# Performance work log

Measured on AMD Instinct MI355X. Metric: run time of the kernel, lower is better.

## Reference

```python
import jax, jax.numpy as jnp
import numpy as np

IN_F = 4096
OUT_F = 4096
N_TOK = 8192
MAX_ITER = IN_F * OUT_F // 2  # default max_iter=-1 -> half of weight entries


def _approx_matmul(x, weight, max_iter):
    """Budgeted approximate matmul: only the `max_iter` largest-magnitude
    weight entries participate (the rest of the multiply-accumulate budget is
    skipped). Faithful to the iteration-budget semantics of Approx_Matmul:
    max_iter multiply-adds out of in_features*out_features total.
    """
    n = weight.size
    flat_abs = jnp.abs(weight).reshape(-1)
    # threshold = k-th largest magnitude (static k -> jit-friendly)
    kth = jnp.sort(flat_abs)[n - max_iter]
    mask = (jnp.abs(weight) >= kth).astype(weight.dtype)
    w_eff = weight * jax.lax.stop_gradient(mask)
    # y[t, o] = sum_i x[t, i] * w_eff[o, i]
    return jnp.einsum('ti,oi->to', x, w_eff)


def setup_inputs() -> dict:
    key = jax.random.key(0)
    kx, kw, kb = jax.random.split(key, 3)
    x = jax.random.normal(kx, (N_TOK, IN_F), dtype=jnp.float32)
    # kaiming_uniform_(a=sqrt(5)) on [out, in] -> bound = 1/sqrt(in_features)
    bound = 1.0 / np.sqrt(IN_F)
    weight = jax.random.uniform(kw, (OUT_F, IN_F), dtype=jnp.float32,
                                minval=-bound, maxval=bound)
    bias = jax.random.uniform(kb, (OUT_F,), dtype=jnp.float32,
                              minval=-bound, maxval=bound)
    return {"x": x, "weight": weight, "bias": bias}


def reference(x, weight, bias):
    mid = _approx_matmul(x, weight, MAX_ITER)
    return mid + bias
```

## Files before the change

### kernel.cpp

```cpp
#include <hip/hip_runtime.h>

#define IN_F   4096
#define OUT_F  4096
#define N_TOK  8192
#define NW     (OUT_F * IN_F)
#define SEL_TARGET 8388608u
#define CAND_CAP (1u << 20)

#define LO_BITS 0x3BFCA000u
#define HI_BITS 0x3C018000u

typedef unsigned int  u32;
typedef unsigned short u16;

typedef __bf16 bf16x8 __attribute__((ext_vector_type(8)));
typedef float  f32x4  __attribute__((ext_vector_type(4)));
typedef u32    u32x4  __attribute__((ext_vector_type(4)));

__device__ inline u16 f2bf_rne(float f) {
    u32 u = __float_as_uint(f);
    u32 r = (u + 0x7fffu + ((u >> 16) & 1u)) >> 16;
    return (u16)r;
}

__global__ __launch_bounds__(256) void front_fused_kernel(
    const uint4* __restrict__ wb, const f32x4* __restrict__ xb,
    u32* __restrict__ cand, u16* __restrict__ x16,
    u32* __restrict__ scal) {
    if (blockIdx.x < 1024) {
        __shared__ u32 lbuf[4096];
        __shared__ u32 lcnt, gbase, lblw;
        if (threadIdx.x == 0) { lcnt = 0; lblw = 0; }
        __syncthreads();

        const int base = blockIdx.x * 4096;
        u32 cntb = 0;
        #pragma unroll 4
        for (int j = 0; j < 16; j++) {
            uint4 v = wb[base + threadIdx.x + j * 256];
            u32 k[4] = {v.x & 0x7fffffffu, v.y & 0x7fffffffu,
                        v.z & 0x7fffffffu, v.w & 0x7fffffffu};
            #pragma unroll
            for (int e = 0; e < 4; e++) {
                u32 kk = k[e];
                cntb += (kk < LO_BITS) ? 1u : 0u;
                if (kk >= LO_BITS && kk < HI_BITS) {
                    u32 idx = atomicAdd(&lcnt, 1u);
                    if (idx < 4096) lbuf[idx] = kk;
                    else scal[6] = 1u;
                }
            }
        }
        #pragma unroll
        for (int off = 32; off; off >>= 1) cntb += __shfl_down(cntb, off);
        if ((threadIdx.x & 63) == 0) atomicAdd(&lblw, cntb);
        __syncthreads();
        if (threadIdx.x == 0) {
            gbase = atomicAdd(&scal[3], min(lcnt, 4096u));
            atomicAdd(&scal[4], lblw);
        }
        __syncthreads();
        const u32 n = min(lcnt, 4096u), gb = gbase;
        for (u32 i = threadIdx.x; i < n; i += 256)
            if (gb + i < CAND_CAP) cand[gb + i] = lbuf[i];
    } else {
        const int stride = 2048 * 256;
        for (int i = (blockIdx.x - 1024) * 256 + threadIdx.x;
             i < (N_TOK * IN_F) / 4; i += stride) {
            f32x4 v = __builtin_nontemporal_load(&xb[i]);
            ushort4 o;
            o.x = f2bf_rne(v.x);
            o.y = f2bf_rne(v.y);
            o.z = f2bf_rne(v.z);
            o.w = f2bf_rne(v.w);
            *(ushort4*)&x16[(size_t)i * 4] = o;
        }
    }
}

#define SCAN1024(part, t)                                            \
    do { _Pragma("unroll")                                           \
        for (int off_ = 1; off_ < 1024; off_ <<= 1) {                \
            u32 v_ = ((t) >= off_) ? part[(t) - off_] : 0u;          \
            __syncthreads();                                         \
            part[t] += v_;                                           \
            __syncthreads();                                         \
        } } while (0)

__global__ __launch_bounds__(1024) void select_win_kernel(const u32* __restrict__ cand,
                                                          const uint4* __restrict__ wb,
                                                          u32* __restrict__ scal) {
    __shared__ u32 h[2048];
    __shared__ u32 part[1024];
    __shared__ u32 sh[2];
    const int t = threadIdx.x;
    const u32 n = scal[3], below = scal[4], ovf = scal[6];
    const bool valid = (n > 0) && (n <= CAND_CAP) && (ovf == 0) &&
                       (below <= SEL_TARGET) && (SEL_TARGET < below + n);

    if (valid) {
        u32 tgt = SEL_TARGET - below;
        const uint4* c4 = (const uint4*)cand;
        const u32 n4 = n >> 2;

        h[t] = 0; h[t + 1024] = 0;
        __syncthreads();
        for (u32 i = t; i < n4; i += 1024) {
            uint4 v = c4[i];
            atomicAdd(&h[(v.x - LO_BITS) >> 9], 1u);
            atomicAdd(&h[(v.y - LO_BITS) >> 9], 1u);
            atomicAdd(&h[(v.z - LO_BITS) >> 9], 1u);
            atomicAdd(&h[(v.w - LO_BITS) >> 9], 1u);
        }
        for (u32 i = (n4 << 2) + t; i < n; i += 1024)
            atomicAdd(&h[(cand[i] - LO_BITS) >> 9], 1u);
        __syncthreads();
        u32 c = h[t];
        part[t] = c;
        __syncthreads();
        SCAN1024(part, t);
        u32 cum = (t == 0) ? 0u : part[t - 1];
        if (tgt >= cum && tgt < cum + c) { sh[0] = (u32)t; sh[1] = tgt - cum; }
        __syncthreads();
        const u32 b1 = sh[0];
        tgt = sh[1];
        __syncthreads();

        h[t] = 0; h[t + 1024] = 0;
        __syncthreads();
        for (u32 i = t; i < n4; i += 1024) {
            uint4 v = c4[i];
            u32 d0 = v.x - LO_BITS, d1 = v.y - LO_BITS,
                d2 = v.z - LO_BITS, d3 = v.w - LO_BITS;
            if ((d0 >> 9) == b1) atomicAdd(&h[d0 & 511u], 1u);
            if ((d1 >> 9) == b1) atomicAdd(&h[d1 & 511u], 1u);
            if ((d2 >> 9) == b1) atomicAdd(&h[d2 & 511u], 1u);
            if ((d3 >> 9) == b1) atomicAdd(&h[d3 & 511u], 1u);
        }
        for (u32 i = (n4 << 2) + t; i < n; i += 1024) {
            u32 d = cand[i] - LO_BITS;
            if ((d >> 9) == b1) atomicAdd(&h[d & 511u], 1u);
        }
        __syncthreads();
        c = (t < 512) ? h[t] : 0u;
        part[t] = c;
        __syncthreads();
        SCAN1024(part, t);
        cum = (t == 0) ? 0u : part[t - 1];
        if (tgt >= cum && tgt < cum + c)
            scal[2] = LO_BITS + (b1 << 9) + (u32)t;
        return;
    }

    u32 tgt = SEL_TARGET;
    const int nvec = NW / 4;
    h[t] = 0; h[t + 1024] = 0;
    __syncthreads();
    for (int i = t; i < nvec; i += 1024) {
        uint4 v = wb[i];
        atomicAdd(&h[(v.x & 0x7fffffffu) >> 20], 1u);
        atomicAdd(&h[(v.y & 0x7fffffffu) >> 20], 1u);
        atomicAdd(&h[(v.z & 0x7fffffffu) >> 20], 1u);
        atomicAdd(&h[(v.w & 0x7fffffffu) >> 20], 1u);
    }
    __syncthreads();
    u32 a0 = h[2 * t], a1 = h[2 * t + 1];
    part[t] = a0 + a1;
    __syncthreads();
    SCAN1024(part, t);
    u32 cum = (t == 0) ? 0u : part[t - 1];
    if (tgt >= cum && tgt < cum + a0) { sh[0] = (u32)(2 * t);     sh[1] = tgt - cum; }
    cum += a0;
    if (tgt >= cum && tgt < cum + a1) { sh[0] = (u32)(2 * t + 1); sh[1] = tgt - cum; }
    __syncthreads();
    const u32 b1f = sh[0];
    tgt = sh[1];
    __syncthreads();

    h[t] = 0; h[t + 1024] = 0;
    __syncthreads();
    for (int i = t; i < nvec; i += 1024) {
        uint4 v = wb[i];
        u32 k[4] = {v.x & 0x7fffffffu, v.y & 0x7fffffffu,
                    v.z & 0x7fffffffu, v.w & 0x7fffffffu};
        #pragma unroll
        for (int e = 0; e < 4; e++)
            if ((k[e] >> 20) == b1f) atomicAdd(&h[(k[e] >> 9) & 2047u], 1u);
    }
    __syncthreads();
    a0 = h[2 * t]; a1 = h[2 * t + 1];
    part[t] = a0 + a1;
    __syncthreads();
    SCAN1024(part, t);
    cum = (t == 0) ? 0u : part[t - 1];
    if (tgt >= cum && tgt < cum + a0) { sh[0] = (u32)(2 * t);     sh[1] = tgt - cum; }
    cum += a0;
    if (tgt >= cum && tgt < cum + a1) { sh[0] = (u32)(2 * t + 1); sh[1] = tgt - cum; }
    __syncthreads();
    const u32 pfx22 = (b1f << 11) | sh[0];
    tgt = sh[1];
    __syncthreads();

    h[t] = 0; h[t + 1024] = 0;
    __syncthreads();
    for (int i = t; i < nvec; i += 1024) {
        uint4 v = wb[i];
        u32 k[4] = {v.x & 0x7fffffffu, v.y & 0x7fffffffu,
                    v.z & 0x7fffffffu, v.w & 0x7fffffffu};
        #pragma unroll
        for (int e = 0; e < 4; e++)
            if ((k[e] >> 9) == pfx22) atomicAdd(&h[k[e] & 511u], 1u);
    }
    __syncthreads();
    u32 c = (t < 512) ? h[t] : 0u;
    part[t] = c;
    __syncthreads();
    SCAN1024(part, t);
    cum = (t == 0) ? 0u : part[t - 1];
    if (tgt >= cum && tgt < cum + c)
        scal[2] = (pfx22 << 9) | (u32)t;
}

__global__ __launch_bounds__(256) void convert_w_kernel(const u32x4* __restrict__ wb,
                                                        u16* __restrict__ w16,
                                                        const u32* __restrict__ scal) {
    const u32 kth = scal[2];
    const int nvec = NW / 4;
    const int stride = gridDim.x * blockDim.x;
    for (int i = blockIdx.x * blockDim.x + threadIdx.x; i < nvec; i += stride) {
        u32x4 v = __builtin_nontemporal_load(&wb[i]);
        ushort4 o;
        o.x = ((v.x & 0x7fffffffu) >= kth) ? f2bf_rne(__uint_as_float(v.x)) : (u16)0;
        o.y = ((v.y & 0x7fffffffu) >= kth) ? f2bf_rne(__uint_as_float(v.y)) : (u16)0;
        o.z = ((v.z & 0x7fffffffu) >= kth) ? f2bf_rne(__uint_as_float(v.z)) : (u16)0;
        o.w = ((v.w & 0x7fffffffu) >= kth) ? f2bf_rne(__uint_as_float(v.w)) : (u16)0;
        *(ushort4*)&w16[(size_t)i * 4] = o;
    }
}

#define BK 64
#define NT (IN_F / BK)

#define ASLOT(buf, ks) (((buf) * 2 + (ks)) * 8192)
#define BSLOT(buf, ks) (32768 + ((buf) * 2 + (ks)) * 8192)

#define VMCNT(n) asm volatile("s_waitcnt vmcnt(" #n ")" ::: "memory")
#define LGKM0    asm volatile("s_waitcnt lgkmcnt(0)" ::: "memory")
#define BARR()   __builtin_amdgcn_s_barrier()

__global__ __launch_bounds__(512, 2) void gemm8p(
    const u16* __restrict__ A,
    const u16* __restrict__ B,
    const float* __restrict__ bias,
    float* __restrict__ C) {
    __shared__ u16 lds[65536];

    const int tid  = threadIdx.x;
    const int lane = tid & 63;
    const int ln15 = lane & 15;
    const int l16  = lane >> 4;
    const int wv   = tid >> 6;
    const int wr   = wv >> 2;
    const int wc   = wv & 3;
    const int wrow = wr * 128;
    const int wcol = wc * 64;

    const int bid = blockIdx.x;
    const int swz = (bid & 7) * 64 + (bid >> 3);
    const int by  = swz >> 4;
    const int bx  = swz & 15;
    const int arow = by * 256;
    const int brow = bx * 256;

    f32x4 acc[8][4];
    #pragma unroll
    for (int m = 0; m < 8; m++)
        #pragma unroll
        for (int n = 0; n < 4; n++)
            acc[m][n] = {0.f, 0.f, 0.f, 0.f};

    #define STAGE(G, rowbase, kt, ks, slot) do {                                        \
        _Pragma("unroll")                                                               \
        for (int i_ = 0; i_ < 2; i_++) {                                                \
            int q_  = tid + i_ * 512;                                                   \
            int r_  = q_ >> 2;                                                          \
            int cs_ = (q_ & 3) ^ ((r_ >> 1) & 3);                                       \
            const u16* src_ = (G) + (size_t)((rowbase) + r_) * IN_F                     \
                              + (kt) * BK + (ks) * 32 + cs_ * 8;                        \
            __builtin_amdgcn_global_load_lds(                                           \
                (const __attribute__((address_space(1))) unsigned int*)src_,            \
                (__attribute__((address_space(3))) unsigned int*)&lds[(slot) + q_ * 8], \
                16, 0, 0);                                                              \
        } } while (0)

    #define READ_A(mh, ks, buf) do {                                                    \
        _Pragma("unroll")                                                               \
        for (int i_ = 0; i_ < 4; i_++) {                                                \
            int row_ = wrow + ((mh) * 4 + i_) * 16 + ln15;                              \
            int cc_  = l16 ^ ((row_ >> 1) & 3);                                         \
            aF[i_] = *(const bf16x8*)&lds[ASLOT(buf, ks) + row_ * 32 + cc_ * 8];        \
        } } while (0)

    #define READ_B(ks, buf) do {                                                       \
        _Pragma("unroll")                                                               \
        for (int i_ = 0; i_ < 4; i_++) {                                                \
            int row_ = wcol + i_ * 16 + ln15;                                           \
            int cc_  = l16 ^ ((row_ >> 1) & 3);                                         \
            bF[i_] = *(const bf16x8*)&lds[BSLOT(buf, ks) + row_ * 32 + cc_ * 8];        \
        } } while (0)

    #define MFMAQ(mh) do {                                                              \
        __builtin_amdgcn_s_setprio(1);                                                  \
        _Pragma("unroll")                                                               \
        for (int i_ = 0; i_ < 4; i_++)                                                  \
            _Pragma("unroll")                                                           \
            for (int n_ = 0; n_ < 4; n_++)                                              \
                acc[(mh) * 4 + i_][n_] = __builtin_amdgcn_mfma_f32_16x16x32_bf16(       \
                    aF[i_], bF[n_], acc[(mh) * 4 + i_][n_], 0, 0, 0);                   \
        __builtin_amdgcn_s_setprio(0);                                                  \
    } while (0)

    STAGE(B, brow, 0, 0, BSLOT(0, 0));
    STAGE(A, arow, 0, 0, ASLOT(0, 0));
    STAGE(B, brow, 0, 1, BSLOT(0, 1));
    STAGE(A, arow, 0, 1, ASLOT(0, 1));
    VMCNT(4);
    STAGE(B, brow, 1, 0, BSLOT(1, 0));
    STAGE(A, arow, 1, 0, ASLOT(1, 0));
    STAGE(B, brow, 1, 1, BSLOT(1, 1));
    VMCNT(6);
    BARR();

    bf16x8 aF[4], bF[4];

    #pragma unroll 1
    for (int it = 0; it < NT / 2; it++) {
        const int t0 = 2 * it;
        const int ka = t0 + 1;
        const int kb = (t0 + 2 < NT) ? t0 + 2 : NT - 1;
        const int kc = (t0 + 3 < NT) ? t0 + 3 : NT - 1;

        READ_A(0, 0, 0); READ_B(0, 0);
        STAGE(A, arow, ka, 1, ASLOT(1, 1));
        BARR(); LGKM0; MFMAQ(0); BARR();
        READ_A(1, 0, 0);
        STAGE(B, brow, kb, 0, BSLOT(0, 0));
        BARR(); LGKM0; MFMAQ(1); BARR();
        READ_A(0, 1, 0); READ_B(1, 0);
        STAGE(A, arow, kb, 0, ASLOT(0, 0));
        BARR(); LGKM0; MFMAQ(0); BARR();
        READ_A(1, 1, 0);
        STAGE(B, brow, kb, 1, BSLOT(0, 1));
        VMCNT(6);
        BARR(); LGKM0; MFMAQ(1); BARR();

        READ_A(0, 0, 1); READ_B(0, 1);
        STAGE(A, arow, kb, 1, ASLOT(0, 1));
        BARR(); LGKM0; MFMAQ(0); BARR();
        READ_A(1, 0, 1);
        STAGE(B, brow, kc, 0, BSLOT(1, 0));
        BARR(); LGKM0; MFMAQ(1); BARR();
        READ_A(0, 1, 1); READ_B(1, 1);
        STAGE(A, arow, kc, 0, ASLOT(1, 0));
        BARR(); LGKM0; MFMAQ(0); BARR();
        READ_A(1, 1, 1);
        STAGE(B, brow, kc, 1, BSLOT(1, 1));
        VMCNT(6);
        BARR(); LGKM0; MFMAQ(1); BARR();
    }
    VMCNT(0);

    const int cr = l16 * 4;
    #pragma unroll
    for (int n = 0; n < 4; n++) {
        int col = brow + wcol + n * 16 + ln15;
        float bv = bias[col];
        #pragma unroll
        for (int m = 0; m < 8; m++) {
            int r0 = arow + wrow + m * 16 + cr;
            #pragma unroll
            for (int j = 0; j < 4; j++) {
                float vv = acc[m][n][j] + bv;
                __builtin_nontemporal_store(vv, &C[(size_t)(r0 + j) * OUT_F + col]);
            }
        }
    }
}

extern "C" void kernel_launch(void* const* d_in, const int* in_sizes, int n_in,
                              void* d_out, int out_size, void* d_ws, size_t ws_size,
                              hipStream_t stream) {
    const float* x    = (const float*)d_in[0];
    const float* w    = (const float*)d_in[1];
    const float* bias = (const float*)d_in[2];
    float* out = (float*)d_out;

    char* ws = (char*)d_ws;
    u32* scal  = (u32*)(ws + 0);
    u16* w16   = (u16*)(ws + 65536);
    u16* x16   = (u16*)(ws + 65536 + (size_t)NW * 2);
    u32* cand  = (u32*)w16;

    hipMemsetAsync(scal, 0, 64, stream);

    front_fused_kernel<<<3072, 256, 0, stream>>>((const uint4*)w, (const f32x4*)x,
                                                 cand, x16, scal);
    select_win_kernel<<<1, 1024, 0, stream>>>(cand, (const uint4*)w, scal);
    convert_w_kernel<<<2048, 256, 0, stream>>>((const u32x4*)w, w16, scal);

    gemm8p<<<512, 512, 0, stream>>>(x16, w16, bias, out);
}
```

Before: 347.6 us.

## Write bf16 weights in front pass, then sparsely zero sub-threshold candidates

```diff
diff --git a/kernel.cpp b/kernel.cpp
--- a/kernel.cpp
+++ b/kernel.cpp
@@ -25,10 +25,12 @@
 
 __global__ __launch_bounds__(256) void front_fused_kernel(
     const uint4* __restrict__ wb, const f32x4* __restrict__ xb,
-    u32* __restrict__ cand, u16* __restrict__ x16,
+    u16* __restrict__ w16, u16* __restrict__ x16,
+    u32* __restrict__ cand, u32* __restrict__ cpos,
     u32* __restrict__ scal) {
     if (blockIdx.x < 1024) {
         __shared__ u32 lbuf[4096];
+        __shared__ u32 lpos[4096];
         __shared__ u32 lcnt, gbase, lblw;
         if (threadIdx.x == 0) { lcnt = 0; lblw = 0; }
         __syncthreads();
@@ -37,19 +39,25 @@
         u32 cntb = 0;
         #pragma unroll 4
         for (int j = 0; j < 16; j++) {
-            uint4 v = wb[base + threadIdx.x + j * 256];
+            const int vi = base + threadIdx.x + j * 256;
+            uint4 v = wb[vi];
             u32 k[4] = {v.x & 0x7fffffffu, v.y & 0x7fffffffu,
                         v.z & 0x7fffffffu, v.w & 0x7fffffffu};
+            u32 r[4] = {v.x, v.y, v.z, v.w};
+            ushort4 o;
+            u16* op = (u16*)&o;
             #pragma unroll
             for (int e = 0; e < 4; e++) {
                 u32 kk = k[e];
                 cntb += (kk < LO_BITS) ? 1u : 0u;
+                op[e] = (kk >= LO_BITS) ? f2bf_rne(__uint_as_float(r[e])) : (u16)0;
                 if (kk >= LO_BITS && kk < HI_BITS) {
                     u32 idx = atomicAdd(&lcnt, 1u);
-                    if (idx < 4096) lbuf[idx] = kk;
+                    if (idx < 4096) { lbuf[idx] = kk; lpos[idx] = (u32)vi * 4u + e; }
                     else scal[6] = 1u;
                 }
             }
+            *(ushort4*)&w16[(size_t)vi * 4] = o;
         }
         #pragma unroll
         for (int off = 32; off; off >>= 1) cntb += __shfl_down(cntb, off);
@@ -62,7 +70,7 @@
         __syncthreads();
         const u32 n = min(lcnt, 4096u), gb = gbase;
         for (u32 i = threadIdx.x; i < n; i += 256)
-            if (gb + i < CAND_CAP) cand[gb + i] = lbuf[i];
+            if (gb + i < CAND_CAP) { cand[gb + i] = lbuf[i]; cpos[gb + i] = lpos[i]; }
     } else {
         const int stride = 2048 * 256;
         for (int i = (blockIdx.x - 1024) * 256 + threadIdx.x;
@@ -152,6 +160,7 @@
         return;
     }
 
+    if (t == 0) scal[7] = 1u;
     u32 tgt = SEL_TARGET;
     const int nvec = NW / 4;
     h[t] = 0; h[t + 1024] = 0;
@@ -221,20 +230,27 @@
         scal[2] = (pfx22 << 9) | (u32)t;
 }
 
-__global__ __launch_bounds__(256) void convert_w_kernel(const u32x4* __restrict__ wb,
-                                                        u16* __restrict__ w16,
-                                                        const u32* __restrict__ scal) {
+__global__ __launch_bounds__(256) void finalize_w_kernel(
+    const u32* __restrict__ cand, const u32* __restrict__ cpos,
+    const u32x4* __restrict__ wb, u16* __restrict__ w16,
+    const u32* __restrict__ scal) {
     const u32 kth = scal[2];
-    const int nvec = NW / 4;
-    const int stride = gridDim.x * blockDim.x;
-    for (int i = blockIdx.x * blockDim.x + threadIdx.x; i < nvec; i += stride) {
-        u32x4 v = __builtin_nontemporal_load(&wb[i]);
-        ushort4 o;
-        o.x = ((v.x & 0x7fffffffu) >= kth) ? f2bf_rne(__uint_as_float(v.x)) : (u16)0;
-        o.y = ((v.y & 0x7fffffffu) >= kth) ? f2bf_rne(__uint_as_float(v.y)) : (u16)0;
-        o.z = ((v.z & 0x7fffffffu) >= kth) ? f2bf_rne(__uint_as_float(v.z)) : (u16)0;
-        o.w = ((v.w & 0x7fffffffu) >= kth) ? f2bf_rne(__uint_as_float(v.w)) : (u16)0;
-        *(ushort4*)&w16[(size_t)i * 4] = o;
+    const u32 stride = gridDim.x * blockDim.x;
+    if (scal[7] == 1u) {
+        const u32 nvec = NW / 4;
+        for (u32 i = blockIdx.x * blockDim.x + threadIdx.x; i < nvec; i += stride) {
+            u32x4 v = __builtin_nontemporal_load(&wb[i]);
+            ushort4 o;
+            o.x = ((v.x & 0x7fffffffu) >= kth) ? f2bf_rne(__uint_as_float(v.x)) : (u16)0;
+            o.y = ((v.y & 0x7fffffffu) >= kth) ? f2bf_rne(__uint_as_float(v.y)) : (u16)0;
+            o.z = ((v.z & 0x7fffffffu) >= kth) ? f2bf_rne(__uint_as_float(v.z)) : (u16)0;
+            o.w = ((v.w & 0x7fffffffu) >= kth) ? f2bf_rne(__uint_as_float(v.w)) : (u16)0;
+            *(ushort4*)&w16[(size_t)i * 4] = o;
+        }
+    } else {
+        const u32 n = min(scal[3], CAND_CAP);
+        for (u32 i = blockIdx.x * blockDim.x + threadIdx.x; i < n; i += stride)
+            if (cand[i] < kth) w16[cpos[i]] = (u16)0;
     }
 }
 
@@ -399,14 +415,16 @@
     u32* scal  = (u32*)(ws + 0);
     u16* w16   = (u16*)(ws + 65536);
     u16* x16   = (u16*)(ws + 65536 + (size_t)NW * 2);
-    u32* cand  = (u32*)w16;
+    u32* cand  = (u32*)out;
+    u32* cpos  = cand + CAND_CAP;
 
     hipMemsetAsync(scal, 0, 64, stream);
 
     front_fused_kernel<<<3072, 256, 0, stream>>>((const uint4*)w, (const f32x4*)x,
-                                                 cand, x16, scal);
+                                                 w16, x16, cand, cpos, scal);
     select_win_kernel<<<1, 1024, 0, stream>>>(cand, (const uint4*)w, scal);
-    convert_w_kernel<<<2048, 256, 0, stream>>>((const u32x4*)w, w16, scal);
+    finalize_w_kernel<<<2048, 256, 0, stream>>>(cand, cpos, (const u32x4*)w,
+                                                w16, scal);
 
     gemm8p<<<512, 512, 0, stream>>>(x16, w16, bias, out);
 }
```

Result: no change. 343.3 us (-1.2%).
